# Optimization experiments

Hardware: AMD Instinct MI355X
Metric: run time of the kernel (lower is better)

The kernel has to match this reference:

```python
import jax, jax.numpy as jnp
import numpy as np

PATCH = 3       # patch_size
PAD = PATCH // 2
ITERS = 5       # iterations
RADIUS = 4      # random_search radius


def get_patches(feats, nnf):
    # feats: [b,c,H,W]; nnf: [b,2,h,w] float coords (row, col)
    # Returns per-pixel patches [b,h,w,P,P,c] gathered at rounded, clipped coords
    b, c, H, W = feats.shape
    fp = jnp.pad(feats, ((0, 0), (0, 0), (PAD, PAD), (PAD, PAD)))
    fp = jnp.transpose(fp, (0, 2, 3, 1))  # [b,H+2p,W+2p,c]
    y = jnp.clip(jnp.round(nnf[:, 0]), 0, H - 1).astype(jnp.int32)  # [b,h,w]
    x = jnp.clip(jnp.round(nnf[:, 1]), 0, W - 1).astype(jnp.int32)
    off = jnp.arange(PATCH)
    yy = y[..., None, None] + off[:, None]   # [b,h,w,P,1] (already offset by PAD in padded frame)
    xx = x[..., None, None] + off[None, :]   # [b,h,w,1,P]
    bi = jnp.arange(b)[:, None, None, None, None]
    return fp[bi, yy, xx]  # [b,h,w,P,P,c]


def patch_distance(ps, pt):
    # SSD over patch and channel dims -> [b,h,w]
    return jnp.sum((ps - pt) ** 2, axis=(3, 4, 5))


def propagate(nnf, source, target, direction):
    shifted = jnp.roll(nnf, direction, axis=3)
    cur_d = patch_distance(get_patches(source, nnf), get_patches(target, nnf))
    shf_d = patch_distance(get_patches(source, shifted), get_patches(target, shifted))
    mask = (shf_d < cur_d)[:, None]  # [b,1,h,w]
    return jnp.where(mask, shifted, nnf)


def random_search(nnf, source, target, key):
    hmax = target.shape[2] - 1  # torch code clamps both coords to H-1
    cur_d = patch_distance(get_patches(source, nnf), get_patches(target, nnf))
    for i in range(RADIUS):
        key, k = jax.random.split(key)
        rand_nnf = jnp.clip(
            nnf + jax.random.normal(k, nnf.shape, nnf.dtype) * (2.0 ** (-i)),
            0.0, float(hmax))
        rand_d = patch_distance(get_patches(source, rand_nnf), get_patches(target, rand_nnf))
        mask = rand_d < cur_d  # [b,h,w]
        nnf = jnp.where(mask[:, None], rand_nnf, nnf)
        cur_d = jnp.where(mask, rand_d, cur_d)
    return nnf


def setup_inputs() -> dict:
    key = jax.random.key(0)
    k1, k2 = jax.random.split(key)
    source = jax.random.normal(k1, (2, 32, 256, 256), dtype=jnp.float32)
    target = jax.random.normal(k2, (2, 32, 256, 256), dtype=jnp.float32)
    return {"source": source, "target": target}


def reference(source, target):
    b, c, h, w = source.shape
    k0 = jax.random.key(1)
    k_init, k_loop = jax.random.split(k0)
    # init_nnf: uniform in [0, H_t-1] x [0, W_t-1]
    nnf = jax.random.uniform(k_init, (b, 2, h, w), dtype=source.dtype)
    scale = jnp.array([target.shape[2] - 1, target.shape[3] - 1], source.dtype)
    nnf = nnf * scale[None, :, None, None]
    for t in range(ITERS):
        nnf = propagate(nnf, source, target, 1)
        nnf = propagate(nnf, source, target, -1)
        nnf = random_search(nnf, source, target, jax.random.fold_in(k_loop, t))
    return nnf
```

## Files before the change

### kernel.cpp

```cpp
#include <hip/hip_runtime.h>
#include <stdint.h>

#define DEVFN __device__ __forceinline__

DEVFN float mulf(float a, float b) {
#pragma clang fp contract(off)
  return a * b;
}
DEVFN float addf(float a, float b) {
#pragma clang fp contract(off)
  return a + b;
}
DEVFN float subf(float a, float b) {
#pragma clang fp contract(off)
  return a - b;
}

DEVFN uint32_t tf_bits32(uint32_t k0, uint32_t k1, uint32_t ctr) {
  uint32_t ks2 = k0 ^ k1 ^ 0x1BD11BDAu;
  uint32_t x0 = k0;
  uint32_t x1 = ctr + k1;
#define TFR(d) { x0 += x1; x1 = (x1 << (d)) | (x1 >> (32 - (d))); x1 ^= x0; }
  TFR(13) TFR(15) TFR(26) TFR(6)
  x0 += k1; x1 += ks2 + 1u;
  TFR(17) TFR(29) TFR(16) TFR(24)
  x0 += ks2; x1 += k0 + 2u;
  TFR(13) TFR(15) TFR(26) TFR(6)
  x0 += k0; x1 += k1 + 3u;
  TFR(17) TFR(29) TFR(16) TFR(24)
  x0 += k1; x1 += ks2 + 4u;
  TFR(13) TFR(15) TFR(26) TFR(6)
  x0 += ks2; x1 += k0 + 5u;
#undef TFR
  return x0 ^ x1;
}

DEVFN float xla_cephes_logf(float in) {
  float xv = fmaxf(in, __uint_as_float(0x00800000u));
  uint32_t bits = __float_as_uint(xv);
  int ei = (int)(bits >> 23) - 126;
  float m = __uint_as_float((bits & 0x007FFFFFu) | 0x3F000000u);
  float e = (float)ei;
  const float SQRTHF = __uint_as_float(0x3F3504F3u);
  bool lt = m < SQRTHF;
  float tmp = lt ? m : 0.0f;
  m = subf(m, 1.0f);
  e = subf(e, lt ? 1.0f : 0.0f);
  m = addf(m, tmp);
  float z = mulf(m, m);
  float y = 7.0376836292E-2f;
  y = addf(mulf(y, m), -1.1514610310E-1f);
  y = addf(mulf(y, m),  1.1676998740E-1f);
  y = addf(mulf(y, m), -1.2420140846E-1f);
  y = addf(mulf(y, m),  1.4249322787E-1f);
  y = addf(mulf(y, m), -1.6668057665E-1f);
  y = addf(mulf(y, m),  2.0000714765E-1f);
  y = addf(mulf(y, m), -2.4999993993E-1f);
  y = addf(mulf(y, m),  3.3333331174E-1f);
  y = mulf(y, m);
  y = mulf(y, z);
  y = addf(y, mulf(e, -2.12194440e-4f));
  y = subf(y, mulf(z, 0.5f));
  m = addf(m, y);
  m = addf(m, mulf(e, 0.693359375f));
  return m;
}

DEVFN float xla_log1pf(float a) {
  float large = xla_cephes_logf(addf(a, 1.0f));
  float small = mulf(addf(mulf(-0.5f, a), 1.0f), a);
  return (fabsf(a) < __uint_as_float(0x38D1B717u)) ? small : large;
}

DEVFN float xla_erfinvf(float u) {
  float nxx = -mulf(u, u);
  float w = -xla_log1pf(nxx);
  float p;
  if (w < 5.0f) {
    float s = subf(w, 2.5f);
    p = 2.81022636e-08f;
    p = addf(mulf(p, s), 3.43273939e-07f);
    p = addf(mulf(p, s), -3.5233877e-06f);
    p = addf(mulf(p, s), -4.39150654e-06f);
    p = addf(mulf(p, s), 0.00021858087f);
    p = addf(mulf(p, s), -0.00125372503f);
    p = addf(mulf(p, s), -0.00417768164f);
    p = addf(mulf(p, s), 0.246640727f);
    p = addf(mulf(p, s), 1.50140941f);
  } else {
    float s = subf(__fsqrt_rn(w), 3.0f);
    p = -0.000200214257f;
    p = addf(mulf(p, s), 0.000100950558f);
    p = addf(mulf(p, s), 0.00134934322f);
    p = addf(mulf(p, s), -0.00367342844f);
    p = addf(mulf(p, s), 0.00573950773f);
    p = addf(mulf(p, s), -0.0076224613f);
    p = addf(mulf(p, s), 0.00943887047f);
    p = addf(mulf(p, s), 1.00167406f);
    p = addf(mulf(p, s), 2.83297682f);
  }
  return mulf(p, u);
}

DEVFN float unitf(uint32_t bits) {
  return subf(__uint_as_float((bits >> 9) | 0x3F800000u), 1.0f);
}

DEVFN float jax_normal(uint32_t bits) {
  float f = unitf(bits);
  const float lo = __uint_as_float(0xBF7FFFFFu);
  float u = fmaxf(lo, addf(mulf(f, 2.0f), lo));
  const float sqrt2 = __uint_as_float(0x3FB504F3u);
  return mulf(sqrt2, xla_erfinvf(u));
}

struct PMKeys {
  uint32_t ki0, ki1;
  uint32_t sk[5][4][2];
};
struct NK { uint32_t k[20][2]; };


__global__ __launch_bounds__(256) void qdiff_kernel(const float* __restrict__ S,
                                                    const float* __restrict__ T,
                                                    float* __restrict__ Q) {
  __shared__ float lds[64 * 33];
  const int t = threadIdx.x;
  const int gid = blockIdx.x;
  const int b = gid >> 10;
  const int y = (gid >> 2) & 255;
  const int x0 = (gid & 3) << 6;
  const int xl = t & 63;
  const int cw = t >> 6;
#pragma unroll
  for (int k = 0; k < 8; ++k) {
    int c = k * 4 + cw;
    size_t o = (size_t)(b * 32 + c) * 65536 + (size_t)y * 256 + x0 + xl;
    float d = subf(S[o], T[o]);
    lds[xl * 33 + c] = mulf(d, d);
  }
  __syncthreads();
  size_t base = (size_t)gid * 2048;
#pragma unroll
  for (int k = 0; k < 2; ++k) {
    int e = t * 4 + k * 1024;
    int px = e >> 5, c = e & 31;
    float4 v;
    v.x = lds[px * 33 + c];
    v.y = lds[px * 33 + c + 1];
    v.z = lds[px * 33 + c + 2];
    v.w = lds[px * 33 + c + 3];
    *(float4*)&Q[base + e] = v;
  }
}

__global__ __launch_bounds__(256) void dsum_kernel(const float* __restrict__ Q,
                                                   float* __restrict__ D) {
  const int x = threadIdx.x;
  const int y = blockIdx.x & 255;
  const int b = blockIdx.x >> 8;
  float acc = 0.0f;
  for (int py = 0; py < 3; ++py) {
    int yy = y + py - 1;
    if (yy < 0 || yy > 255) continue;
    for (int px = 0; px < 3; ++px) {
      int xx = x + px - 1;
      if (xx < 0 || xx > 255) continue;
      const float4* p = (const float4*)&Q[((size_t)b * 65536 + yy * 256 + xx) * 32];
      float4 v0 = p[0], v1 = p[1], v2 = p[2], v3 = p[3];
      float4 v4 = p[4], v5 = p[5], v6 = p[6], v7 = p[7];
      acc = addf(acc, v0.x); acc = addf(acc, v0.y); acc = addf(acc, v0.z); acc = addf(acc, v0.w);
      acc = addf(acc, v1.x); acc = addf(acc, v1.y); acc = addf(acc, v1.z); acc = addf(acc, v1.w);
      acc = addf(acc, v2.x); acc = addf(acc, v2.y); acc = addf(acc, v2.z); acc = addf(acc, v2.w);
      acc = addf(acc, v3.x); acc = addf(acc, v3.y); acc = addf(acc, v3.z); acc = addf(acc, v3.w);
      acc = addf(acc, v4.x); acc = addf(acc, v4.y); acc = addf(acc, v4.z); acc = addf(acc, v4.w);
      acc = addf(acc, v5.x); acc = addf(acc, v5.y); acc = addf(acc, v5.z); acc = addf(acc, v5.w);
      acc = addf(acc, v6.x); acc = addf(acc, v6.y); acc = addf(acc, v6.z); acc = addf(acc, v6.w);
      acc = addf(acc, v7.x); acc = addf(acc, v7.y); acc = addf(acc, v7.z); acc = addf(acc, v7.w);
    }
  }
  D[blockIdx.x * 256 + x] = acc;
}

__global__ __launch_bounds__(256) void normals_kernel(float* __restrict__ N, NK K) {
  uint32_t g = blockIdx.x * 256 + threadIdx.x;
  uint32_t ts = g >> 18;
  uint32_t idx = g & 262143u;
  N[g] = jax_normal(tf_bits32(K.k[ts][0], K.k[ts][1], idx));
}

__global__ __launch_bounds__(256) void pm_fast(const float* __restrict__ D,
                                               const float* __restrict__ N,
                                               float* __restrict__ out,
                                               uint32_t ki0, uint32_t ki1) {
  const int j = threadIdx.x;
  const int bb = blockIdx.x >> 8;
  const int i = blockIdx.x & 255;
  const float* Db = D + bb * 65536;
  __shared__ float sy[256], sx[256];

  const uint32_t idx_y = (uint32_t)(bb * 131072 + i * 256 + j);
  const uint32_t idx_x = idx_y + 65536u;

  float nyv[20], nxv[20];
#pragma unroll
  for (int ts = 0; ts < 20; ++ts) {
    nyv[ts] = N[(size_t)ts * 262144 + idx_y];
    nxv[ts] = N[(size_t)ts * 262144 + idx_x];
  }

  float y = mulf(unitf(tf_bits32(ki0, ki1, idx_y)), 255.0f);
  float x = mulf(unitf(tf_bits32(ki0, ki1, idx_x)), 255.0f);

  auto lookup = [&](float yy, float xx) -> float {
    int iy = (int)rintf(yy);
    int ix = (int)rintf(xx);
    iy = min(max(iy, 0), 255);
    ix = min(max(ix, 0), 255);
    return Db[iy * 256 + ix];
  };

  float curd = lookup(y, x);
#pragma unroll
  for (int t = 0; t < 5; ++t) {
    sy[j] = y; sx[j] = x;
    __syncthreads();
    {
      int jn = (j + 255) & 255;
      float yn = sy[jn], xn = sx[jn];
      float shf = lookup(yn, xn);
      if (shf < curd) { y = yn; x = xn; curd = shf; }
    }
    __syncthreads();
    sy[j] = y; sx[j] = x;
    __syncthreads();
    {
      int jn = (j + 1) & 255;
      float yn = sy[jn], xn = sx[jn];
      float shf = lookup(yn, xn);
      if (shf < curd) { y = yn; x = xn; curd = shf; }
    }
    __syncthreads();
    float sigma = 1.0f;
#pragma unroll
    for (int s = 0; s < 4; ++s) {
      float ry = fminf(fmaxf(addf(y, mulf(nyv[t * 4 + s], sigma)), 0.0f), 255.0f);
      float rx = fminf(fmaxf(addf(x, mulf(nxv[t * 4 + s], sigma)), 0.0f), 255.0f);
      float rd = lookup(ry, rx);
      if (rd < curd) { y = ry; x = rx; curd = rd; }
      sigma *= 0.5f;
    }
  }
  out[idx_y] = y;
  out[idx_x] = x;
}


__global__ __launch_bounds__(256) void compute_d(const float* __restrict__ S,
                                                 const float* __restrict__ T,
                                                 float* __restrict__ D) {
  const int x = threadIdx.x;
  const int y = blockIdx.x & 255;
  const int b = blockIdx.x >> 8;
  const int chs = 65536;
  const float* Sb = S + (size_t)b * 32 * chs;
  const float* Tb = T + (size_t)b * 32 * chs;
  float acc = 0.0f;
  for (int py = 0; py < 3; ++py) {
    int yy = y + py - 1;
    if (yy < 0 || yy > 255) continue;
    for (int px = 0; px < 3; ++px) {
      int xx = x + px - 1;
      if (xx < 0 || xx > 255) continue;
      int off = yy * 256 + xx;
      for (int c = 0; c < 32; ++c) {
        float d = subf(Sb[c * chs + off], Tb[c * chs + off]);
        acc = addf(acc, mulf(d, d));
      }
    }
  }
  D[b * chs + y * 256 + x] = acc;
}

__global__ __launch_bounds__(256) void pm_kernel(const float* __restrict__ D,
                                                 float* __restrict__ out,
                                                 PMKeys K) {
  const int j = threadIdx.x;
  const int bb = blockIdx.x >> 8;
  const int i = blockIdx.x & 255;
  const float* Db = D + bb * 65536;
  __shared__ float sy[256], sx[256];

  const uint32_t idx_y = (uint32_t)(bb * 131072 + i * 256 + j);
  const uint32_t idx_x = idx_y + 65536u;

  float y = mulf(unitf(tf_bits32(K.ki0, K.ki1, idx_y)), 255.0f);
  float x = mulf(unitf(tf_bits32(K.ki0, K.ki1, idx_x)), 255.0f);

  auto lookup = [&](float yy, float xx) -> float {
    int iy = (int)rintf(yy);
    int ix = (int)rintf(xx);
    iy = min(max(iy, 0), 255);
    ix = min(max(ix, 0), 255);
    return Db[iy * 256 + ix];
  };

  for (int t = 0; t < 5; ++t) {
    sy[j] = y; sx[j] = x;
    __syncthreads();
    {
      int jn = (j + 255) & 255;
      float yn = sy[jn], xn = sx[jn];
      float cur = lookup(y, x);
      float shf = lookup(yn, xn);
      if (shf < cur) { y = yn; x = xn; }
    }
    __syncthreads();
    sy[j] = y; sx[j] = x;
    __syncthreads();
    {
      int jn = (j + 1) & 255;
      float yn = sy[jn], xn = sx[jn];
      float cur = lookup(y, x);
      float shf = lookup(yn, xn);
      if (shf < cur) { y = yn; x = xn; }
    }
    __syncthreads();
    float cur = lookup(y, x);
    float sigma = 1.0f;
    for (int s = 0; s < 4; ++s) {
      uint32_t kk0 = K.sk[t][s][0], kk1 = K.sk[t][s][1];
      float ny = jax_normal(tf_bits32(kk0, kk1, idx_y));
      float nx = jax_normal(tf_bits32(kk0, kk1, idx_x));
      float ry = fminf(fmaxf(addf(y, mulf(ny, sigma)), 0.0f), 255.0f);
      float rx = fminf(fmaxf(addf(x, mulf(nx, sigma)), 0.0f), 255.0f);
      float rd = lookup(ry, rx);
      if (rd < cur) { y = ry; x = rx; cur = rd; }
      sigma *= 0.5f;
    }
  }
  out[idx_y] = y;
  out[idx_x] = x;
}

static void h_tf(uint32_t k0, uint32_t k1, uint32_t x0, uint32_t x1,
                 uint32_t& o0, uint32_t& o1) {
  uint32_t ks2 = k0 ^ k1 ^ 0x1BD11BDAu;
  x0 += k0; x1 += k1;
#define HR(d) { x0 += x1; x1 = (x1 << (d)) | (x1 >> (32 - (d))); x1 ^= x0; }
  HR(13) HR(15) HR(26) HR(6)
  x0 += k1; x1 += ks2 + 1u;
  HR(17) HR(29) HR(16) HR(24)
  x0 += ks2; x1 += k0 + 2u;
  HR(13) HR(15) HR(26) HR(6)
  x0 += k0; x1 += k1 + 3u;
  HR(17) HR(29) HR(16) HR(24)
  x0 += k1; x1 += ks2 + 4u;
  HR(13) HR(15) HR(26) HR(6)
  x0 += ks2; x1 += k0 + 5u;
#undef HR
  o0 = x0; o1 = x1;
}

extern "C" void kernel_launch(void* const* d_in, const int* in_sizes, int n_in,
                              void* d_out, int out_size, void* d_ws, size_t ws_size,
                              hipStream_t stream) {
  const float* S = (const float*)d_in[0];
  const float* T = (const float*)d_in[1];
  float* out = (float*)d_out;

  PMKeys K;
  uint32_t kl0, kl1;
  h_tf(0u, 1u, 0u, 0u, K.ki0, K.ki1);
  h_tf(0u, 1u, 0u, 1u, kl0, kl1);
  for (uint32_t t = 0; t < 5; ++t) {
    uint32_t c0, c1;
    h_tf(kl0, kl1, 0u, t, c0, c1);
    for (int s = 0; s < 4; ++s) {
      uint32_t n0, n1, s0, s1;
      h_tf(c0, c1, 0u, 0u, n0, n1);
      h_tf(c0, c1, 0u, 1u, s0, s1);
      K.sk[t][s][0] = s0; K.sk[t][s][1] = s1;
      c0 = n0; c1 = n1;
    }
  }

  const size_t D_BYTES = 2ull * 65536 * 4;
  const size_t QN_BYTES = 20ull * 262144 * 4;
  const size_t NEED = D_BYTES + QN_BYTES;

  if (ws_size >= NEED) {
    float* Dd = (float*)d_ws;
    float* QN = (float*)((char*)d_ws + D_BYTES);
    NK nk;
    for (int t = 0; t < 5; ++t)
      for (int s = 0; s < 4; ++s) {
        nk.k[t * 4 + s][0] = K.sk[t][s][0];
        nk.k[t * 4 + s][1] = K.sk[t][s][1];
      }
    hipLaunchKernelGGL(qdiff_kernel, dim3(2048), dim3(256), 0, stream, S, T, QN);
    hipLaunchKernelGGL(dsum_kernel, dim3(512), dim3(256), 0, stream, QN, Dd);
    hipLaunchKernelGGL(normals_kernel, dim3(20480), dim3(256), 0, stream, QN, nk);
    hipLaunchKernelGGL(pm_fast, dim3(512), dim3(256), 0, stream, Dd, QN, out, K.ki0, K.ki1);
  } else {
    float* Dd = (float*)d_ws;
    hipLaunchKernelGGL(compute_d, dim3(512), dim3(256), 0, stream, S, T, Dd);
    hipLaunchKernelGGL(pm_kernel, dim3(512), dim3(256), 0, stream, Dd, out, K);
  }
}
```

Before: 127.6 us.

## Fuse normals generation into qdiff, speculate random-search lookups, swizzle dsum blocks

Normal-sample generation moves into the qdiff kernel, issued between the S/T loads and their use so the RNG arithmetic can hide global memory latency, and one launch is removed. Q and N now get separate workspace buffers instead of sharing one, which raises the workspace requirement. The random-search step evaluates all 15 possible candidate positions up front and picks the accepted path with selects, so the four dependent D lookups become independent loads at the cost of more gathers and registers. dsum blocks are remapped with a swizzle, aimed at better cache locality across concurrently running blocks.

```diff
diff --git a/kernel.cpp b/kernel.cpp
--- a/kernel.cpp
+++ b/kernel.cpp
@@ -120,10 +120,23 @@
 };
 struct NK { uint32_t k[20][2]; };
 
-
-__global__ __launch_bounds__(256) void qdiff_kernel(const float* __restrict__ S,
-                                                    const float* __restrict__ T,
-                                                    float* __restrict__ Q) {
+DEVFN float candf(float base, float n, float sig) {
+  return fminf(fmaxf(addf(base, mulf(n, sig)), 0.0f), 255.0f);
+}
+DEVFN int addr_of(float yy, float xx) {
+  int iy = (int)rintf(yy);
+  int ix = (int)rintf(xx);
+  iy = min(max(iy, 0), 255);
+  ix = min(max(ix, 0), 255);
+  return iy * 256 + ix;
+}
+
+
+__global__ __launch_bounds__(256) void qdiff_n(const float* __restrict__ S,
+                                               const float* __restrict__ T,
+                                               float* __restrict__ Q,
+                                               float* __restrict__ N,
+                                               NK nk) {
   __shared__ float lds[64 * 33];
   const int t = threadIdx.x;
   const int gid = blockIdx.x;
@@ -132,11 +145,29 @@
   const int x0 = (gid & 3) << 6;
   const int xl = t & 63;
   const int cw = t >> 6;
+
+  float sv[8], tv[8];
 #pragma unroll
   for (int k = 0; k < 8; ++k) {
     int c = k * 4 + cw;
     size_t o = (size_t)(b * 32 + c) * 65536 + (size_t)y * 256 + x0 + xl;
-    float d = subf(S[o], T[o]);
+    sv[k] = S[o];
+    tv[k] = T[o];
+  }
+
+  uint32_t gtid = (uint32_t)gid * 256u + (uint32_t)t;
+#pragma unroll
+  for (int i = 0; i < 10; ++i) {
+    uint32_t L = (uint32_t)i * 524288u + gtid;
+    uint32_t ts = L >> 18;
+    uint32_t idx = L & 262143u;
+    N[L] = jax_normal(tf_bits32(nk.k[ts][0], nk.k[ts][1], idx));
+  }
+
+#pragma unroll
+  for (int k = 0; k < 8; ++k) {
+    int c = k * 4 + cw;
+    float d = subf(sv[k], tv[k]);
     lds[xl * 33 + c] = mulf(d, d);
   }
   __syncthreads();
@@ -157,8 +188,10 @@
 __global__ __launch_bounds__(256) void dsum_kernel(const float* __restrict__ Q,
                                                    float* __restrict__ D) {
   const int x = threadIdx.x;
-  const int y = blockIdx.x & 255;
-  const int b = blockIdx.x >> 8;
+  const int bid = blockIdx.x;
+  const int swz = (bid & 7) * 64 + (bid >> 3);
+  const int y = swz & 255;
+  const int b = swz >> 8;
   float acc = 0.0f;
   for (int py = 0; py < 3; ++py) {
     int yy = y + py - 1;
@@ -179,14 +212,7 @@
       acc = addf(acc, v7.x); acc = addf(acc, v7.y); acc = addf(acc, v7.z); acc = addf(acc, v7.w);
     }
   }
-  D[blockIdx.x * 256 + x] = acc;
-}
-
-__global__ __launch_bounds__(256) void normals_kernel(float* __restrict__ N, NK K) {
-  uint32_t g = blockIdx.x * 256 + threadIdx.x;
-  uint32_t ts = g >> 18;
-  uint32_t idx = g & 262143u;
-  N[g] = jax_normal(tf_bits32(K.k[ts][0], K.k[ts][1], idx));
+  D[(b * 256 + y) * 256 + x] = acc;
 }
 
 __global__ __launch_bounds__(256) void pm_fast(const float* __restrict__ D,
@@ -212,15 +238,7 @@
   float y = mulf(unitf(tf_bits32(ki0, ki1, idx_y)), 255.0f);
   float x = mulf(unitf(tf_bits32(ki0, ki1, idx_x)), 255.0f);
 
-  auto lookup = [&](float yy, float xx) -> float {
-    int iy = (int)rintf(yy);
-    int ix = (int)rintf(xx);
-    iy = min(max(iy, 0), 255);
-    ix = min(max(ix, 0), 255);
-    return Db[iy * 256 + ix];
-  };
-
-  float curd = lookup(y, x);
+  float curd = Db[addr_of(y, x)];
 #pragma unroll
   for (int t = 0; t < 5; ++t) {
     sy[j] = y; sx[j] = x;
@@ -228,7 +246,7 @@
     {
       int jn = (j + 255) & 255;
       float yn = sy[jn], xn = sx[jn];
-      float shf = lookup(yn, xn);
+      float shf = Db[addr_of(yn, xn)];
       if (shf < curd) { y = yn; x = xn; curd = shf; }
     }
     __syncthreads();
@@ -237,19 +255,69 @@
     {
       int jn = (j + 1) & 255;
       float yn = sy[jn], xn = sx[jn];
-      float shf = lookup(yn, xn);
+      float shf = Db[addr_of(yn, xn)];
       if (shf < curd) { y = yn; x = xn; curd = shf; }
     }
     __syncthreads();
-    float sigma = 1.0f;
-#pragma unroll
-    for (int s = 0; s < 4; ++s) {
-      float ry = fminf(fmaxf(addf(y, mulf(nyv[t * 4 + s], sigma)), 0.0f), 255.0f);
-      float rx = fminf(fmaxf(addf(x, mulf(nxv[t * 4 + s], sigma)), 0.0f), 255.0f);
-      float rd = lookup(ry, rx);
-      if (rd < curd) { y = ry; x = rx; curd = rd; }
-      sigma *= 0.5f;
-    }
+
+    float n0y = nyv[t * 4 + 0], n0x = nxv[t * 4 + 0];
+    float n1y = nyv[t * 4 + 1], n1x = nxv[t * 4 + 1];
+    float n2y = nyv[t * 4 + 2], n2x = nxv[t * 4 + 2];
+    float n3y = nyv[t * 4 + 3], n3x = nxv[t * 4 + 3];
+
+    float c0y = candf(y, n0y, 1.0f),  c0x = candf(x, n0x, 1.0f);
+    float c1Ay = candf(y,   n1y, 0.5f), c1Ax = candf(x,   n1x, 0.5f);
+    float c1By = candf(c0y, n1y, 0.5f), c1Bx = candf(c0x, n1x, 0.5f);
+    float c2_0y = candf(y,    n2y, 0.25f), c2_0x = candf(x,    n2x, 0.25f);
+    float c2_1y = candf(c1Ay, n2y, 0.25f), c2_1x = candf(c1Ax, n2x, 0.25f);
+    float c2_2y = candf(c0y,  n2y, 0.25f), c2_2x = candf(c0x,  n2x, 0.25f);
+    float c2_3y = candf(c1By, n2y, 0.25f), c2_3x = candf(c1Bx, n2x, 0.25f);
+    float c3_0y = candf(y,     n3y, 0.125f), c3_0x = candf(x,     n3x, 0.125f);
+    float c3_1y = candf(c2_0y, n3y, 0.125f), c3_1x = candf(c2_0x, n3x, 0.125f);
+    float c3_2y = candf(c1Ay,  n3y, 0.125f), c3_2x = candf(c1Ax,  n3x, 0.125f);
+    float c3_3y = candf(c2_1y, n3y, 0.125f), c3_3x = candf(c2_1x, n3x, 0.125f);
+    float c3_4y = candf(c0y,   n3y, 0.125f), c3_4x = candf(c0x,   n3x, 0.125f);
+    float c3_5y = candf(c2_2y, n3y, 0.125f), c3_5x = candf(c2_2x, n3x, 0.125f);
+    float c3_6y = candf(c1By,  n3y, 0.125f), c3_6x = candf(c1Bx,  n3x, 0.125f);
+    float c3_7y = candf(c2_3y, n3y, 0.125f), c3_7x = candf(c2_3x, n3x, 0.125f);
+
+    float d0   = Db[addr_of(c0y,  c0x)];
+    float d1A  = Db[addr_of(c1Ay, c1Ax)];
+    float d1B  = Db[addr_of(c1By, c1Bx)];
+    float d2_0 = Db[addr_of(c2_0y, c2_0x)];
+    float d2_1 = Db[addr_of(c2_1y, c2_1x)];
+    float d2_2 = Db[addr_of(c2_2y, c2_2x)];
+    float d2_3 = Db[addr_of(c2_3y, c2_3x)];
+    float d3_0 = Db[addr_of(c3_0y, c3_0x)];
+    float d3_1 = Db[addr_of(c3_1y, c3_1x)];
+    float d3_2 = Db[addr_of(c3_2y, c3_2x)];
+    float d3_3 = Db[addr_of(c3_3y, c3_3x)];
+    float d3_4 = Db[addr_of(c3_4y, c3_4x)];
+    float d3_5 = Db[addr_of(c3_5y, c3_5x)];
+    float d3_6 = Db[addr_of(c3_6y, c3_6x)];
+    float d3_7 = Db[addr_of(c3_7y, c3_7x)];
+
+    bool a0 = d0 < curd;
+    y = a0 ? c0y : y;  x = a0 ? c0x : x;  curd = a0 ? d0 : curd;
+
+    float s1y = a0 ? c1By : c1Ay, s1x = a0 ? c1Bx : c1Ax, s1d = a0 ? d1B : d1A;
+    bool a1 = s1d < curd;
+    y = a1 ? s1y : y;  x = a1 ? s1x : x;  curd = a1 ? s1d : curd;
+
+    float s2y = a0 ? (a1 ? c2_3y : c2_2y) : (a1 ? c2_1y : c2_0y);
+    float s2x = a0 ? (a1 ? c2_3x : c2_2x) : (a1 ? c2_1x : c2_0x);
+    float s2d = a0 ? (a1 ? d2_3 : d2_2) : (a1 ? d2_1 : d2_0);
+    bool a2 = s2d < curd;
+    y = a2 ? s2y : y;  x = a2 ? s2x : x;  curd = a2 ? s2d : curd;
+
+    float s3y = a0 ? (a1 ? (a2 ? c3_7y : c3_6y) : (a2 ? c3_5y : c3_4y))
+                   : (a1 ? (a2 ? c3_3y : c3_2y) : (a2 ? c3_1y : c3_0y));
+    float s3x = a0 ? (a1 ? (a2 ? c3_7x : c3_6x) : (a2 ? c3_5x : c3_4x))
+                   : (a1 ? (a2 ? c3_3x : c3_2x) : (a2 ? c3_1x : c3_0x));
+    float s3d = a0 ? (a1 ? (a2 ? d3_7 : d3_6) : (a2 ? d3_5 : d3_4))
+                   : (a1 ? (a2 ? d3_3 : d3_2) : (a2 ? d3_1 : d3_0));
+    bool a3 = s3d < curd;
+    y = a3 ? s3y : y;  x = a3 ? s3x : x;  curd = a3 ? s3d : curd;
   }
   out[idx_y] = y;
   out[idx_x] = x;
@@ -386,22 +454,23 @@
   }
 
   const size_t D_BYTES = 2ull * 65536 * 4;
-  const size_t QN_BYTES = 20ull * 262144 * 4;
-  const size_t NEED = D_BYTES + QN_BYTES;
+  const size_t Q_BYTES = 2ull * 65536 * 32 * 4;
+  const size_t N_BYTES = 20ull * 262144 * 4;
+  const size_t NEED = D_BYTES + Q_BYTES + N_BYTES;
 
   if (ws_size >= NEED) {
     float* Dd = (float*)d_ws;
-    float* QN = (float*)((char*)d_ws + D_BYTES);
+    float* Qq = (float*)((char*)d_ws + D_BYTES);
+    float* Nn = (float*)((char*)d_ws + D_BYTES + Q_BYTES);
     NK nk;
     for (int t = 0; t < 5; ++t)
       for (int s = 0; s < 4; ++s) {
         nk.k[t * 4 + s][0] = K.sk[t][s][0];
         nk.k[t * 4 + s][1] = K.sk[t][s][1];
       }
-    hipLaunchKernelGGL(qdiff_kernel, dim3(2048), dim3(256), 0, stream, S, T, QN);
-    hipLaunchKernelGGL(dsum_kernel, dim3(512), dim3(256), 0, stream, QN, Dd);
-    hipLaunchKernelGGL(normals_kernel, dim3(20480), dim3(256), 0, stream, QN, nk);
-    hipLaunchKernelGGL(pm_fast, dim3(512), dim3(256), 0, stream, Dd, QN, out, K.ki0, K.ki1);
+    hipLaunchKernelGGL(qdiff_n, dim3(2048), dim3(256), 0, stream, S, T, Qq, Nn, nk);
+    hipLaunchKernelGGL(dsum_kernel, dim3(512), dim3(256), 0, stream, Qq, Dd);
+    hipLaunchKernelGGL(pm_fast, dim3(512), dim3(256), 0, stream, Dd, Nn, out, K.ki0, K.ki1);
   } else {
     float* Dd = (float*)d_ws;
     hipLaunchKernelGGL(compute_d, dim3(512), dim3(256), 0, stream, S, T, Dd);
```

Measured after the change: 127.4 us. No clear change (-0.2%).
